# Kernel tuning notes

Measured on AMD Instinct MI355X. Metric: run time of the kernel, lower is better.

## Reference

```python
import jax, jax.numpy as jnp
import numpy as np

N_NODES = 100000
N_EDGES = 800000
EDGE_NAMES = ["ei_connected_to", "ei_ordered_next", "ei_represents", "ei_represented_by",
              "ei_neighboring_vertical", "ei_neighboring_horizontal", "ei_contains",
              "ei_order", "ei_perpendicular"]
AGGRS_L2 = ["sum", "sum", "mean", "mean", "sum", "sum", "mean"]


def _glorot(key, shape):
    fan_in, fan_out = shape[-2], shape[-1]
    s = (2.0 / (fan_in + fan_out)) ** 0.5
    return jax.random.normal(key, shape, dtype=jnp.float32) * s


def setup_inputs() -> dict:
    key = jax.random.key(0)
    ks = iter(jax.random.split(key, 32))
    inp = {"x": jax.random.normal(next(ks), (N_NODES, 6), dtype=jnp.float32)}
    for name in EDGE_NAMES:
        inp[name] = jax.random.randint(next(ks), (2, N_EDGES), 0, N_NODES, dtype=jnp.int32)
    inp.update(
        W0n=_glorot(next(ks), (2, 6, 16)), W0r=_glorot(next(ks), (2, 6, 16)),
        b0=jnp.zeros((2, 16), jnp.float32),
        W1n=_glorot(next(ks), (2, 16, 32)), W1r=_glorot(next(ks), (2, 16, 32)),
        b1=jnp.zeros((2, 32), jnp.float32),
        P1=_glorot(next(ks), (16, 32)), pb1=jnp.zeros((32,), jnp.float32),
        W2n=_glorot(next(ks), (7, 32, 64)), W2r=_glorot(next(ks), (7, 32, 64)),
        b2=jnp.zeros((7, 64), jnp.float32),
        P2=_glorot(next(ks), (32, 64)), pb2=jnp.zeros((64,), jnp.float32),
    )
    return inp


def _hetero_conv(x, edges, aggrs, Wn, Wr, b):
    # Per-relation GraphConv: out_d = aggr(x[src]->dst) @ Wn_r + x @ Wr_r + b_r,
    # summed across relations (HeteroConv aggr='sum'). Loop is over a small fixed
    # set of relation types (structurally distinct), not data dims.
    n = x.shape[0]
    out = jnp.zeros((n, Wn.shape[-1]), x.dtype)
    for i, (ei, aggr) in enumerate(zip(edges, aggrs)):
        src, dst = ei[0], ei[1]
        msg = jax.ops.segment_sum(x[src], dst, num_segments=n)  # scatter-add gather
        if aggr == "mean":
            cnt = jax.ops.segment_sum(jnp.ones_like(dst, dtype=x.dtype), dst, num_segments=n)
            msg = msg / jnp.maximum(cnt, 1.0)[:, None]
        out = out + msg @ Wn[i] + x @ Wr[i] + b[i]
    return out


def reference(x, W0n, W0r, b0, W1n, W1r, b1, P1, pb1, W2n, W2r, b2, P2, pb2,
              ei_connected_to, ei_ordered_next, ei_represents, ei_represented_by,
              ei_neighboring_vertical, ei_neighboring_horizontal, ei_contains,
              ei_order, ei_perpendicular):
    e01 = [ei_connected_to, ei_ordered_next]
    e2 = [ei_represents, ei_represented_by, ei_neighboring_vertical,
          ei_neighboring_horizontal, ei_contains, ei_order, ei_perpendicular]
    # local head: 6 -> 16 (two sum relations)
    h = _hetero_conv(x, e01, ["sum", "sum"], W0n, W0r, b0)
    # residual block 1: 16 -> 32 (same two sum relations, linear residual projection)
    h = jax.nn.relu(_hetero_conv(h, e01, ["sum", "sum"], W1n, W1r, b1) + h @ P1 + pb1)
    # residual block 2: 32 -> 64 (seven relations, sum/mean aggregation)
    h = jax.nn.relu(_hetero_conv(h, e2, AGGRS_L2, W2n, W2r, b2) + h @ P2 + pb2)
    # final elementwise relu from SemanticModule.forward
    return jax.nn.relu(h)
```

## Files before the change

### kernel.cpp

```cpp
#include <hip/hip_runtime.h>

#define NN 100000
#define NE 800000
#define NRG 256
#define SPAN 392
#define CAP 4096
#define NBIN (9 * NRG)

typedef _Float16 f16;
typedef __attribute__((ext_vector_type(4))) _Float16 f16x4;
typedef __attribute__((ext_vector_type(8))) _Float16 f16x8;
typedef __attribute__((ext_vector_type(4))) float f32x4;
typedef __attribute__((ext_vector_type(2))) float f32x2;

#define NTL(p) __builtin_nontemporal_load(p)

struct EPtrs { const int* s[9]; const int* d[9]; };

__global__ __launch_bounds__(256) void prep_weights(
    const float* __restrict__ W0n, const float* __restrict__ W0r, const float* __restrict__ b0,
    const float* __restrict__ W1n, const float* __restrict__ W1r, const float* __restrict__ b1,
    const float* __restrict__ P1,  const float* __restrict__ pb1,
    const float* __restrict__ W2n, const float* __restrict__ W2r, const float* __restrict__ b2,
    const float* __restrict__ P2,  const float* __restrict__ pb2,
    float* __restrict__ wc0, float* __restrict__ bc0,
    float* __restrict__ wc1, float* __restrict__ bc1,
    f16*   __restrict__ b2frag, float* __restrict__ bc2,
    int*   __restrict__ cursor)
{
    int gtid = blockIdx.x * 256 + threadIdx.x;
    int gstr = gridDim.x * 256;

    for (int t = gtid; t < NBIN; t += gstr) cursor[t] = 0;

    for (int t = gtid; t < 18 * 16; t += gstr) {
        int row = t >> 4, col = t & 15;
        float v;
        if (row < 6)       v = W0n[row * 16 + col];
        else if (row < 12) v = W0n[96 + (row - 6) * 16 + col];
        else               v = W0r[(row - 12) * 16 + col] + W0r[96 + (row - 12) * 16 + col];
        wc0[t] = v;
    }
    for (int t = gtid; t < 16; t += gstr) bc0[t] = b0[t] + b0[16 + t];

    for (int t = gtid; t < 48 * 32; t += gstr) {
        int row = t >> 5, col = t & 31;
        float v;
        if (row < 16)      v = W1n[row * 32 + col];
        else if (row < 32) v = W1n[512 + (row - 16) * 32 + col];
        else { int rr = row - 32; v = W1r[rr * 32 + col] + W1r[512 + rr * 32 + col] + P1[rr * 32 + col]; }
        wc1[t] = v;
    }
    for (int t = gtid; t < 32; t += gstr) bc1[t] = b1[t] + b1[32 + t] + pb1[t];

    for (int t = gtid; t < 256 * 64; t += gstr) {
        int j = t & 7, lane = (t >> 3) & 63, ntk = t >> 9;
        int nt = ntk & 3, kt = ntk >> 2;
        int k = kt * 32 + (lane >> 4) * 8 + j;
        int n = nt * 16 + (lane & 15);
        float v;
        if (k < 224) v = W2n[k * 64 + n];
        else {
            int rr = k - 224;
            v = P2[rr * 64 + n];
            #pragma unroll
            for (int r = 0; r < 7; ++r) v += W2r[r * 2048 + rr * 64 + n];
        }
        b2frag[t] = (f16)v;
    }
    for (int t = gtid; t < 64; t += gstr) {
        float v = pb2[t];
        #pragma unroll
        for (int r = 0; r < 7; ++r) v += b2[r * 64 + t];
        bc2[t] = v;
    }
}

__global__ __launch_bounds__(256) void passA(EPtrs ep, int* __restrict__ cursor,
                                             unsigned* __restrict__ binbuf)
{
    int r = blockIdx.y;
    int e0 = blockIdx.x * 4096;
    int cnt = min(4096, NE - e0);
    int tid = threadIdx.x;
    __shared__ int h[NRG];
    __shared__ int bs[NRG];
    __shared__ int cl[NRG];
    __shared__ int gb[NRG];
    __shared__ int wsumA[4];
    __shared__ unsigned pk[4096];
    __shared__ unsigned char pkb[4096];

    h[tid] = 0;
    __syncthreads();

    const int* dp = ep.d[r];
    const int* sp = ep.s[r];
    unsigned wv[16];
    int rgk[16];
    #pragma unroll
    for (int k = 0; k < 16; ++k) {
        int e = e0 + k * 256 + tid;
        rgk[k] = -1;
        if (e < NE) {
            int d = NTL(dp + e);
            int sv = NTL(sp + e);
            int g = d / SPAN;
            int l = d - g * SPAN;
            wv[k] = ((unsigned)l << 17) | (unsigned)sv;
            rgk[k] = g;
            atomicAdd(&h[g], 1);
        }
    }
    __syncthreads();

    int vcnt = h[tid];
    int lane = tid & 63, wid = tid >> 6;
    int incl = vcnt;
    #pragma unroll
    for (int ofs = 1; ofs < 64; ofs <<= 1) {
        int u = __shfl_up(incl, ofs, 64);
        if (lane >= ofs) incl += u;
    }
    if (lane == 63) wsumA[wid] = incl;
    __syncthreads();
    if (tid == 0) {
        int a = wsumA[0], b = wsumA[1], c = wsumA[2];
        wsumA[0] = 0; wsumA[1] = a; wsumA[2] = a + b; wsumA[3] = a + b + c;
    }
    __syncthreads();
    int excl = incl - vcnt + wsumA[wid];
    bs[tid] = excl;
    cl[tid] = excl;
    gb[tid] = (vcnt > 0) ? atomicAdd(&cursor[r * NRG + tid], vcnt) : 0;
    __syncthreads();

    #pragma unroll
    for (int k = 0; k < 16; ++k) {
        if (rgk[k] >= 0) {
            int p = atomicAdd(&cl[rgk[k]], 1);
            pk[p] = wv[k];
            pkb[p] = (unsigned char)rgk[k];
        }
    }
    __syncthreads();

    for (int i = tid; i < cnt; i += 256) {
        int g = pkb[i];
        int pos = gb[g] + (i - bs[g]);
        if (pos < CAP)
            binbuf[((size_t)(r * NRG + g)) * CAP + pos] = pk[i];
    }
}

__global__ __launch_bounds__(256) void passB(const unsigned* __restrict__ binbuf,
                                             const int* __restrict__ cursor,
                                             int* __restrict__ deg, int* __restrict__ off,
                                             int* __restrict__ eidx)
{
    int bin = blockIdx.x;
    int r = bin >> 8, rg = bin & (NRG - 1);
    int lo = rg * SPAN;
    int n_here = min(SPAN, NN - lo);
    int tid = threadIdx.x;
    __shared__ int h[SPAN];
    __shared__ int wsum[4];
    __shared__ int stage[CAP];

    int sz = min(cursor[bin], CAP);
    const unsigned* bp = binbuf + (size_t)bin * CAP;

    for (int i = tid; i < SPAN; i += 256) h[i] = 0;
    __syncthreads();

    unsigned wv[16];
    int rk[16];
    #pragma unroll
    for (int k = 0; k < 16; ++k) {
        int e = tid + k * 256;
        if (e < sz) {
            unsigned w = NTL(bp + e);
            wv[k] = w;
            rk[k] = atomicAdd(&h[w >> 17], 1);
        }
    }
    __syncthreads();

    int i0 = tid * 2;
    int dstash[2];
    int s = 0;
    #pragma unroll
    for (int k = 0; k < 2; ++k) {
        int i = i0 + k;
        int v = (i < SPAN) ? h[i] : 0;
        dstash[k] = v;
        s += v;
    }
    int lane = tid & 63, wid = tid >> 6;
    int incl = s;
    #pragma unroll
    for (int ofs = 1; ofs < 64; ofs <<= 1) {
        int u = __shfl_up(incl, ofs, 64);
        if (lane >= ofs) incl += u;
    }
    if (lane == 63) wsum[wid] = incl;
    __syncthreads();
    if (tid == 0) {
        int a = wsum[0], b = wsum[1], c = wsum[2];
        wsum[0] = 0; wsum[1] = a; wsum[2] = a + b; wsum[3] = a + b + c;
    }
    __syncthreads();
    int run = incl - s + wsum[wid];
    int base = bin * CAP;
    #pragma unroll
    for (int k = 0; k < 2; ++k) {
        int i = i0 + k;
        if (i < SPAN) {
            int v = dstash[k];
            h[i] = run;
            if (i < n_here) {
                deg[r * NN + lo + i] = v;
                off[r * NN + lo + i] = base + run + v;
            }
            run += v;
        }
    }
    __syncthreads();

    #pragma unroll
    for (int k = 0; k < 16; ++k) {
        int e = tid + k * 256;
        if (e < sz) {
            unsigned w = wv[k];
            stage[h[w >> 17] + rk[k]] = (int)(w & 0x1FFFF);
        }
    }
    __syncthreads();
    for (int i = tid; i < sz; i += 256) eidx[base + i] = stage[i];
}

__global__ __launch_bounds__(256) void t0f(const float* __restrict__ x,
                                           const int* __restrict__ deg, const int* __restrict__ off,
                                           const int* __restrict__ eidx,
                                           const float* __restrict__ wc0, const float* __restrict__ bc0,
                                           f16* __restrict__ h0h)
{
    __shared__ float sw[288 + 16];
    for (int t = threadIdx.x; t < 304; t += 256) sw[t] = (t < 288) ? wc0[t] : bc0[t - 288];
    __syncthreads();
    int t = blockIdx.x * 256 + threadIdx.x;
    int node = t >> 2;
    if (node >= NN) return;
    int l = t & 3;
    int r = l >> 1, p = l & 1;

    float m[6] = {0, 0, 0, 0, 0, 0};
    {
        int e1 = off[r * NN + node];
        int e0 = e1 - deg[r * NN + node];
        int e = e0 + p;
        for (; e + 2 < e1; e += 4) {
            int sA = eidx[e], sB = eidx[e + 2];
            const float2* pA = reinterpret_cast<const float2*>(x + (size_t)sA * 6);
            const float2* pB = reinterpret_cast<const float2*>(x + (size_t)sB * 6);
            float2 a0 = pA[0], a1 = pA[1], a2 = pA[2];
            float2 b0 = pB[0], b1 = pB[1], b2 = pB[2];
            m[0] += a0.x + b0.x; m[1] += a0.y + b0.y;
            m[2] += a1.x + b1.x; m[3] += a1.y + b1.y;
            m[4] += a2.x + b2.x; m[5] += a2.y + b2.y;
        }
        if (e < e1) {
            int sA = eidx[e];
            const float2* pA = reinterpret_cast<const float2*>(x + (size_t)sA * 6);
            float2 a0 = pA[0], a1 = pA[1], a2 = pA[2];
            m[0] += a0.x; m[1] += a0.y; m[2] += a1.x; m[3] += a1.y; m[4] += a2.x; m[5] += a2.y;
        }
    }
    float mo[6];
    #pragma unroll
    for (int k = 0; k < 6; ++k) {
        m[k] += __shfl_xor(m[k], 1, 64);
        mo[k] = __shfl_xor(m[k], 2, 64);
    }
    int baseOwn = r * 96, baseOth = (1 - r) * 96;
    float xv[6];
    {
        const float2* xp = reinterpret_cast<const float2*>(x + (size_t)node * 6);
        float2 a = xp[0], b = xp[1], c = xp[2];
        xv[0] = a.x; xv[1] = a.y; xv[2] = b.x; xv[3] = b.y; xv[4] = c.x; xv[5] = c.y;
    }
    int dc = l * 4;
    float acc[4];
    #pragma unroll
    for (int j = 0; j < 4; ++j) acc[j] = sw[288 + dc + j];
    #pragma unroll
    for (int k = 0; k < 6; ++k) {
        #pragma unroll
        for (int j = 0; j < 4; ++j) {
            acc[j] = fmaf(m[k],  sw[baseOwn + k * 16 + dc + j], acc[j]);
            acc[j] = fmaf(mo[k], sw[baseOth + k * 16 + dc + j], acc[j]);
            acc[j] = fmaf(xv[k], sw[192 + k * 16 + dc + j], acc[j]);
        }
    }
    f16x4 o;
    #pragma unroll
    for (int j = 0; j < 4; ++j) o[j] = (f16)acc[j];
    *reinterpret_cast<f16x4*>(h0h + (size_t)node * 16 + dc) = o;
}

__global__ __launch_bounds__(256) void g1t(const int* __restrict__ deg, const int* __restrict__ off,
                                           const int* __restrict__ eidx, const f16* __restrict__ h0h,
                                           const float* __restrict__ wc1, const float* __restrict__ bc1,
                                           f16* __restrict__ h1h, unsigned* __restrict__ h1q)
{
    __shared__ float sw[1536 + 32];
    __shared__ float ms[32][33];
    for (int t = threadIdx.x; t < 1568; t += 256) sw[t] = (t < 1536) ? wc1[t] : bc1[t - 1536];

    int tid = threadIdx.x;
    int nloc = tid >> 3, l = tid & 7;
    int r = l >> 2, dq = l & 3;
    int node = blockIdx.x * 32 + nloc;

    if (node < NN) {
        int e1 = off[r * NN + node];
        int e0 = e1 - deg[r * NN + node];
        float a0 = 0.f, a1 = 0.f, a2 = 0.f, a3 = 0.f;
        int e = e0;
        for (; e + 4 <= e1; e += 4) {
            int sA = eidx[e], sB = eidx[e + 1], sC = eidx[e + 2], sD = eidx[e + 3];
            f16x4 vA = *reinterpret_cast<const f16x4*>(h0h + (size_t)sA * 16 + dq * 4);
            f16x4 vB = *reinterpret_cast<const f16x4*>(h0h + (size_t)sB * 16 + dq * 4);
            f16x4 vC = *reinterpret_cast<const f16x4*>(h0h + (size_t)sC * 16 + dq * 4);
            f16x4 vD = *reinterpret_cast<const f16x4*>(h0h + (size_t)sD * 16 + dq * 4);
            a0 += (float)vA[0] + (float)vB[0] + (float)vC[0] + (float)vD[0];
            a1 += (float)vA[1] + (float)vB[1] + (float)vC[1] + (float)vD[1];
            a2 += (float)vA[2] + (float)vB[2] + (float)vC[2] + (float)vD[2];
            a3 += (float)vA[3] + (float)vB[3] + (float)vC[3] + (float)vD[3];
        }
        for (; e < e1; ++e) {
            f16x4 v = *reinterpret_cast<const f16x4*>(h0h + (size_t)eidx[e] * 16 + dq * 4);
            a0 += (float)v[0]; a1 += (float)v[1]; a2 += (float)v[2]; a3 += (float)v[3];
        }
        ms[nloc][r * 16 + dq * 4 + 0] = a0;
        ms[nloc][r * 16 + dq * 4 + 1] = a1;
        ms[nloc][r * 16 + dq * 4 + 2] = a2;
        ms[nloc][r * 16 + dq * 4 + 3] = a3;
    }
    __syncthreads();
    if (node >= NN) return;

    int c0 = l * 4;
    float acc[4];
    #pragma unroll
    for (int j = 0; j < 4; ++j) acc[j] = sw[1536 + c0 + j];
    #pragma unroll
    for (int k = 0; k < 32; ++k) {
        float s = ms[nloc][k];
        #pragma unroll
        for (int j = 0; j < 4; ++j) acc[j] = fmaf(s, sw[k * 32 + c0 + j], acc[j]);
    }
    {
        const f16x8* hp = reinterpret_cast<const f16x8*>(h0h + (size_t)node * 16);
        f16x8 a = hp[0], b = hp[1];
        #pragma unroll
        for (int k = 0; k < 8; ++k) {
            float s0 = (float)a[k], s1 = (float)b[k];
            #pragma unroll
            for (int j = 0; j < 4; ++j)
                acc[j] = fmaf(s0, sw[(32 + k) * 32 + c0 + j], fmaf(s1, sw[(40 + k) * 32 + c0 + j], acc[j]));
        }
    }
    #pragma unroll
    for (int j = 0; j < 4; ++j) acc[j] = fmaxf(acc[j], 0.f);

    f16x4 o;
    #pragma unroll
    for (int j = 0; j < 4; ++j) o[j] = (f16)acc[j];
    *reinterpret_cast<f16x4*>(h1h + (size_t)node * 32 + c0) = o;

    int w0 = __builtin_amdgcn_cvt_pk_fp8_f32(acc[0], acc[1], 0, false);
    w0 = __builtin_amdgcn_cvt_pk_fp8_f32(acc[2], acc[3], w0, true);
    h1q[(size_t)node * 8 + l] = (unsigned)w0;
}

__global__ __launch_bounds__(256, 8) void g2t2(const int* __restrict__ deg, const int* __restrict__ off,
                                               const int* __restrict__ eidx, const unsigned* __restrict__ h1q,
                                               const f16* __restrict__ h1h, const f16* __restrict__ b2frag,
                                               const float* __restrict__ bc2, float* __restrict__ out)
{
    __shared__ f16 cat[16][264];

    int tid = threadIdx.x;
    int nloc = tid >> 4;
    int lane16 = tid & 15;
    int node = blockIdx.x * 16 + nloc;

    if (lane16 >= 14) {
        int part = lane16 - 14;
        const f16x8* hp = reinterpret_cast<const f16x8*>(h1h + (size_t)node * 32 + part * 16);
        f16x8 v0 = hp[0], v1 = hp[1];
        *reinterpret_cast<f16x8*>(&cat[nloc][224 + part * 16]) = v0;
        *reinterpret_cast<f16x8*>(&cat[nloc][224 + part * 16 + 8]) = v1;
    } else {
        int r = lane16 >> 1;
        int half = lane16 & 1;
        int d = deg[(r + 2) * NN + node];
        int e1 = off[(r + 2) * NN + node];
        int e0 = e1 - d;

        f32x2 acc[8];
        #pragma unroll
        for (int q = 0; q < 8; ++q) acc[q] = (f32x2){0.f, 0.f};

        const uint4* tbl = reinterpret_cast<const uint4*>(h1q);
        int e = e0;
        for (; e + 2 <= e1; e += 2) {
            int sA = eidx[e], sB = eidx[e + 1];
            uint4 qA = tbl[(size_t)sA * 2 + half];
            uint4 qB = tbl[(size_t)sB * 2 + half];
            acc[0] += __builtin_amdgcn_cvt_pk_f32_fp8(qA.x, false);
            acc[1] += __builtin_amdgcn_cvt_pk_f32_fp8(qA.x, true);
            acc[2] += __builtin_amdgcn_cvt_pk_f32_fp8(qA.y, false);
            acc[3] += __builtin_amdgcn_cvt_pk_f32_fp8(qA.y, true);
            acc[4] += __builtin_amdgcn_cvt_pk_f32_fp8(qA.z, false);
            acc[5] += __builtin_amdgcn_cvt_pk_f32_fp8(qA.z, true);
            acc[6] += __builtin_amdgcn_cvt_pk_f32_fp8(qA.w, false);
            acc[7] += __builtin_amdgcn_cvt_pk_f32_fp8(qA.w, true);
            acc[0] += __builtin_amdgcn_cvt_pk_f32_fp8(qB.x, false);
            acc[1] += __builtin_amdgcn_cvt_pk_f32_fp8(qB.x, true);
            acc[2] += __builtin_amdgcn_cvt_pk_f32_fp8(qB.y, false);
            acc[3] += __builtin_amdgcn_cvt_pk_f32_fp8(qB.y, true);
            acc[4] += __builtin_amdgcn_cvt_pk_f32_fp8(qB.z, false);
            acc[5] += __builtin_amdgcn_cvt_pk_f32_fp8(qB.z, true);
            acc[6] += __builtin_amdgcn_cvt_pk_f32_fp8(qB.w, false);
            acc[7] += __builtin_amdgcn_cvt_pk_f32_fp8(qB.w, true);
        }
        if (e < e1) {
            int sA = eidx[e];
            uint4 qA = tbl[(size_t)sA * 2 + half];
            acc[0] += __builtin_amdgcn_cvt_pk_f32_fp8(qA.x, false);
            acc[1] += __builtin_amdgcn_cvt_pk_f32_fp8(qA.x, true);
            acc[2] += __builtin_amdgcn_cvt_pk_f32_fp8(qA.y, false);
            acc[3] += __builtin_amdgcn_cvt_pk_f32_fp8(qA.y, true);
            acc[4] += __builtin_amdgcn_cvt_pk_f32_fp8(qA.z, false);
            acc[5] += __builtin_amdgcn_cvt_pk_f32_fp8(qA.z, true);
            acc[6] += __builtin_amdgcn_cvt_pk_f32_fp8(qA.w, false);
            acc[7] += __builtin_amdgcn_cvt_pk_f32_fp8(qA.w, true);
        }

        float sc = (r == 2 || r == 3 || r == 6) ? (1.0f / (float)max(d, 1)) : 1.0f;
        f16x8 o0, o1;
        #pragma unroll
        for (int q = 0; q < 4; ++q) {
            o0[q * 2 + 0] = (f16)(acc[q][0] * sc);
            o0[q * 2 + 1] = (f16)(acc[q][1] * sc);
            o1[q * 2 + 0] = (f16)(acc[4 + q][0] * sc);
            o1[q * 2 + 1] = (f16)(acc[4 + q][1] * sc);
        }
        *reinterpret_cast<f16x8*>(&cat[nloc][r * 32 + half * 16]) = o0;
        *reinterpret_cast<f16x8*>(&cat[nloc][r * 32 + half * 16 + 8]) = o1;
    }

    int lane = tid & 63, w = tid >> 6;
    int quad = lane >> 4, col0 = lane & 15;
    float bcv = bc2[w * 16 + col0];

    f16x8 bfr[8];
    #pragma unroll
    for (int kt = 0; kt < 8; ++kt)
        bfr[kt] = *reinterpret_cast<const f16x8*>(b2frag + ((size_t)(kt * 4 + w) * 64 + lane) * 8);

    __syncthreads();

    f32x4 acc = (f32x4){0.f, 0.f, 0.f, 0.f};
    #pragma unroll
    for (int kt = 0; kt < 8; ++kt) {
        f16x8 a = *reinterpret_cast<const f16x8*>(&cat[col0][kt * 32 + quad * 8]);
        acc = __builtin_amdgcn_mfma_f32_16x16x32_f16(a, bfr[kt], acc, 0, 0, 0);
    }

    int row0 = blockIdx.x * 16 + quad * 4;
    #pragma unroll
    for (int i = 0; i < 4; ++i)
        out[(size_t)(row0 + i) * 64 + w * 16 + col0] = fmaxf(acc[i] + bcv, 0.f);
}

extern "C" void kernel_launch(void* const* d_in, const int* in_sizes, int n_in,
                              void* d_out, int out_size, void* d_ws, size_t ws_size,
                              hipStream_t stream)
{
    const float* x = (const float*)d_in[0];
    EPtrs ep;
    for (int i = 0; i < 9; ++i) { const int* p = (const int*)d_in[1 + i]; ep.s[i] = p; ep.d[i] = p + NE; }
    const float* W0n = (const float*)d_in[10]; const float* W0r = (const float*)d_in[11];
    const float* b0  = (const float*)d_in[12];
    const float* W1n = (const float*)d_in[13]; const float* W1r = (const float*)d_in[14];
    const float* b1  = (const float*)d_in[15];
    const float* P1  = (const float*)d_in[16]; const float* pb1 = (const float*)d_in[17];
    const float* W2n = (const float*)d_in[18]; const float* W2r = (const float*)d_in[19];
    const float* b2  = (const float*)d_in[20];
    const float* P2  = (const float*)d_in[21]; const float* pb2 = (const float*)d_in[22];
    float* out = (float*)d_out;
    char* ws = (char*)d_ws;

    size_t off_b = 0;
    auto alloc = [&](size_t b) { size_t o = off_b; off_b += (b + 255) & ~(size_t)255; return o; };
    size_t o_wc0 = alloc(288 * 4);   size_t o_bc0 = alloc(16 * 4);
    size_t o_wc1 = alloc(1536 * 4);  size_t o_bc1 = alloc(32 * 4);
    size_t o_b2f = alloc(16384 * 2); size_t o_bc2 = alloc(64 * 4);
    size_t o_h0h = alloc((size_t)NN * 16 * 2);
    size_t o_h1q = alloc((size_t)NN * 32);
    size_t o_h1h = alloc((size_t)NN * 32 * 2);
    size_t o_bin = alloc((size_t)NBIN * CAP * 4);
    size_t o_deg = alloc((size_t)9 * NN * 4);
    size_t o_off = alloc((size_t)9 * NN * 4);
    size_t o_eid = alloc((size_t)NBIN * CAP * 4);
    size_t o_cur = alloc((size_t)NBIN * 4);
    (void)ws_size;

    float* wc0 = (float*)(ws + o_wc0); float* bc0 = (float*)(ws + o_bc0);
    float* wc1 = (float*)(ws + o_wc1); float* bc1 = (float*)(ws + o_bc1);
    f16*   b2f = (f16*)(ws + o_b2f);   float* bc2 = (float*)(ws + o_bc2);
    f16*   h0h = (f16*)(ws + o_h0h);
    unsigned* h1q = (unsigned*)(ws + o_h1q);
    f16*   h1h = (f16*)(ws + o_h1h);
    unsigned* binbuf = (unsigned*)(ws + o_bin);
    int*   deg = (int*)(ws + o_deg);
    int*   offp = (int*)(ws + o_off);
    int*   eid = (int*)(ws + o_eid);
    int*   cur = (int*)(ws + o_cur);

    dim3 B(256);
    prep_weights<<<32, B, 0, stream>>>(W0n, W0r, b0, W1n, W1r, b1, P1, pb1,
                                       W2n, W2r, b2, P2, pb2,
                                       wc0, bc0, wc1, bc1, b2f, bc2, cur);
    passA<<<dim3((NE + 4095) / 4096, 9), B, 0, stream>>>(ep, cur, binbuf);
    passB<<<NBIN, B, 0, stream>>>(binbuf, cur, deg, offp, eid);

    t0f<<<(NN * 4 + 255) / 256, B, 0, stream>>>(x, deg, offp, eid, wc0, bc0, h0h);
    g1t<<<(NN + 31) / 32, B, 0, stream>>>(deg, offp, eid, h0h, wc1, bc1, h1h, h1q);
    g2t2<<<NN / 16, B, 0, stream>>>(deg, offp, eid, h1q, h1h, b2f, bc2, out);
}
```

Baseline: 281.1 us.

## Split g1t gather across lane pairs, drop passA second atomic, split g2t2 launch

passA now keeps the rank returned by the histogram atomic and uses it for placement, removing the second round of shared atomics and the cl array. g1t assigns 16 threads per node instead of 8: each pair of lanes splits one relation's edge list, and the pair combines its partial sums with a shuffle, so each node's gather runs with more parallel loads. g1t now uses 16 nodes per block and computes 2 output columns per thread, with fp8 packing done through a shuffle. g2t2 is launched as two half-size grids over node ranges, adding a base-offset parameter; this adds a launch and gives no clear benefit.

```diff
diff --git a/kernel.cpp b/kernel.cpp
--- a/kernel.cpp
+++ b/kernel.cpp
@@ -8,6 +8,7 @@
 #define NBIN (9 * NRG)
 
 typedef _Float16 f16;
+typedef __attribute__((ext_vector_type(2))) _Float16 f16x2;
 typedef __attribute__((ext_vector_type(4))) _Float16 f16x4;
 typedef __attribute__((ext_vector_type(8))) _Float16 f16x8;
 typedef __attribute__((ext_vector_type(4))) float f32x4;
@@ -85,7 +86,6 @@
     int tid = threadIdx.x;
     __shared__ int h[NRG];
     __shared__ int bs[NRG];
-    __shared__ int cl[NRG];
     __shared__ int gb[NRG];
     __shared__ int wsumA[4];
     __shared__ unsigned pk[4096];
@@ -98,6 +98,7 @@
     const int* sp = ep.s[r];
     unsigned wv[16];
     int rgk[16];
+    int lrk[16];
     #pragma unroll
     for (int k = 0; k < 16; ++k) {
         int e = e0 + k * 256 + tid;
@@ -109,7 +110,7 @@
             int l = d - g * SPAN;
             wv[k] = ((unsigned)l << 17) | (unsigned)sv;
             rgk[k] = g;
-            atomicAdd(&h[g], 1);
+            lrk[k] = atomicAdd(&h[g], 1);
         }
     }
     __syncthreads();
@@ -131,14 +132,13 @@
     __syncthreads();
     int excl = incl - vcnt + wsumA[wid];
     bs[tid] = excl;
-    cl[tid] = excl;
     gb[tid] = (vcnt > 0) ? atomicAdd(&cursor[r * NRG + tid], vcnt) : 0;
     __syncthreads();
 
     #pragma unroll
     for (int k = 0; k < 16; ++k) {
         if (rgk[k] >= 0) {
-            int p = atomicAdd(&cl[rgk[k]], 1);
+            int p = bs[rgk[k]] + lrk[k];
             pk[p] = wv[k];
             pkb[p] = (unsigned char)rgk[k];
         }
@@ -314,51 +314,52 @@
                                            f16* __restrict__ h1h, unsigned* __restrict__ h1q)
 {
     __shared__ float sw[1536 + 32];
-    __shared__ float ms[32][33];
+    __shared__ float ms[16][33];
     for (int t = threadIdx.x; t < 1568; t += 256) sw[t] = (t < 1536) ? wc1[t] : bc1[t - 1536];
 
     int tid = threadIdx.x;
-    int nloc = tid >> 3, l = tid & 7;
-    int r = l >> 2, dq = l & 3;
-    int node = blockIdx.x * 32 + nloc;
-
-    if (node < NN) {
+    int nloc = tid >> 4, l = tid & 15;
+    int r = l >> 3, dq = (l >> 1) & 3, p = l & 1;
+    int node = blockIdx.x * 16 + nloc;
+
+    {
         int e1 = off[r * NN + node];
         int e0 = e1 - deg[r * NN + node];
         float a0 = 0.f, a1 = 0.f, a2 = 0.f, a3 = 0.f;
-        int e = e0;
-        for (; e + 4 <= e1; e += 4) {
-            int sA = eidx[e], sB = eidx[e + 1], sC = eidx[e + 2], sD = eidx[e + 3];
+        int e = e0 + p;
+        for (; e + 2 < e1; e += 4) {
+            int sA = eidx[e], sB = eidx[e + 2];
             f16x4 vA = *reinterpret_cast<const f16x4*>(h0h + (size_t)sA * 16 + dq * 4);
             f16x4 vB = *reinterpret_cast<const f16x4*>(h0h + (size_t)sB * 16 + dq * 4);
-            f16x4 vC = *reinterpret_cast<const f16x4*>(h0h + (size_t)sC * 16 + dq * 4);
-            f16x4 vD = *reinterpret_cast<const f16x4*>(h0h + (size_t)sD * 16 + dq * 4);
-            a0 += (float)vA[0] + (float)vB[0] + (float)vC[0] + (float)vD[0];
-            a1 += (float)vA[1] + (float)vB[1] + (float)vC[1] + (float)vD[1];
-            a2 += (float)vA[2] + (float)vB[2] + (float)vC[2] + (float)vD[2];
-            a3 += (float)vA[3] + (float)vB[3] + (float)vC[3] + (float)vD[3];
-        }
-        for (; e < e1; ++e) {
+            a0 += (float)vA[0] + (float)vB[0];
+            a1 += (float)vA[1] + (float)vB[1];
+            a2 += (float)vA[2] + (float)vB[2];
+            a3 += (float)vA[3] + (float)vB[3];
+        }
+        if (e < e1) {
             f16x4 v = *reinterpret_cast<const f16x4*>(h0h + (size_t)eidx[e] * 16 + dq * 4);
             a0 += (float)v[0]; a1 += (float)v[1]; a2 += (float)v[2]; a3 += (float)v[3];
         }
-        ms[nloc][r * 16 + dq * 4 + 0] = a0;
-        ms[nloc][r * 16 + dq * 4 + 1] = a1;
-        ms[nloc][r * 16 + dq * 4 + 2] = a2;
-        ms[nloc][r * 16 + dq * 4 + 3] = a3;
-    }
-    __syncthreads();
-    if (node >= NN) return;
-
-    int c0 = l * 4;
-    float acc[4];
-    #pragma unroll
-    for (int j = 0; j < 4; ++j) acc[j] = sw[1536 + c0 + j];
+        a0 += __shfl_xor(a0, 1, 64);
+        a1 += __shfl_xor(a1, 1, 64);
+        a2 += __shfl_xor(a2, 1, 64);
+        a3 += __shfl_xor(a3, 1, 64);
+        if (p == 0) {
+            ms[nloc][r * 16 + dq * 4 + 0] = a0;
+            ms[nloc][r * 16 + dq * 4 + 1] = a1;
+            ms[nloc][r * 16 + dq * 4 + 2] = a2;
+            ms[nloc][r * 16 + dq * 4 + 3] = a3;
+        }
+    }
+    __syncthreads();
+
+    int c0 = l * 2;
+    float acc0 = sw[1536 + c0], acc1 = sw[1536 + c0 + 1];
     #pragma unroll
     for (int k = 0; k < 32; ++k) {
         float s = ms[nloc][k];
-        #pragma unroll
-        for (int j = 0; j < 4; ++j) acc[j] = fmaf(s, sw[k * 32 + c0 + j], acc[j]);
+        acc0 = fmaf(s, sw[k * 32 + c0], acc0);
+        acc1 = fmaf(s, sw[k * 32 + c0 + 1], acc1);
     }
     {
         const f16x8* hp = reinterpret_cast<const f16x8*>(h0h + (size_t)node * 16);
@@ -366,35 +367,38 @@
         #pragma unroll
         for (int k = 0; k < 8; ++k) {
             float s0 = (float)a[k], s1 = (float)b[k];
-            #pragma unroll
-            for (int j = 0; j < 4; ++j)
-                acc[j] = fmaf(s0, sw[(32 + k) * 32 + c0 + j], fmaf(s1, sw[(40 + k) * 32 + c0 + j], acc[j]));
-        }
-    }
-    #pragma unroll
-    for (int j = 0; j < 4; ++j) acc[j] = fmaxf(acc[j], 0.f);
-
-    f16x4 o;
-    #pragma unroll
-    for (int j = 0; j < 4; ++j) o[j] = (f16)acc[j];
-    *reinterpret_cast<f16x4*>(h1h + (size_t)node * 32 + c0) = o;
-
-    int w0 = __builtin_amdgcn_cvt_pk_fp8_f32(acc[0], acc[1], 0, false);
-    w0 = __builtin_amdgcn_cvt_pk_fp8_f32(acc[2], acc[3], w0, true);
-    h1q[(size_t)node * 8 + l] = (unsigned)w0;
+            acc0 = fmaf(s0, sw[(32 + k) * 32 + c0], fmaf(s1, sw[(40 + k) * 32 + c0], acc0));
+            acc1 = fmaf(s0, sw[(32 + k) * 32 + c0 + 1], fmaf(s1, sw[(40 + k) * 32 + c0 + 1], acc1));
+        }
+    }
+    acc0 = fmaxf(acc0, 0.f);
+    acc1 = fmaxf(acc1, 0.f);
+
+    f16x2 o;
+    o[0] = (f16)acc0; o[1] = (f16)acc1;
+    *reinterpret_cast<f16x2*>(h1h + (size_t)node * 32 + c0) = o;
+
+    float pa0 = __shfl_xor(acc0, 1, 64);
+    float pa1 = __shfl_xor(acc1, 1, 64);
+    if (p == 0) {
+        int w = __builtin_amdgcn_cvt_pk_fp8_f32(acc0, acc1, 0, false);
+        w = __builtin_amdgcn_cvt_pk_fp8_f32(pa0, pa1, w, true);
+        h1q[(size_t)node * 8 + (l >> 1)] = (unsigned)w;
+    }
 }
 
 __global__ __launch_bounds__(256, 8) void g2t2(const int* __restrict__ deg, const int* __restrict__ off,
                                                const int* __restrict__ eidx, const unsigned* __restrict__ h1q,
                                                const f16* __restrict__ h1h, const f16* __restrict__ b2frag,
-                                               const float* __restrict__ bc2, float* __restrict__ out)
+                                               const float* __restrict__ bc2, float* __restrict__ out,
+                                               int nbase)
 {
     __shared__ f16 cat[16][264];
 
     int tid = threadIdx.x;
     int nloc = tid >> 4;
     int lane16 = tid & 15;
-    int node = blockIdx.x * 16 + nloc;
+    int node = nbase + blockIdx.x * 16 + nloc;
 
     if (lane16 >= 14) {
         int part = lane16 - 14;
@@ -480,7 +484,7 @@
         acc = __builtin_amdgcn_mfma_f32_16x16x32_f16(a, bfr[kt], acc, 0, 0, 0);
     }
 
-    int row0 = blockIdx.x * 16 + quad * 4;
+    int row0 = nbase + blockIdx.x * 16 + quad * 4;
     #pragma unroll
     for (int i = 0; i < 4; ++i)
         out[(size_t)(row0 + i) * 64 + w * 16 + col0] = fmaxf(acc[i] + bcv, 0.f);
@@ -539,6 +543,7 @@
     passB<<<NBIN, B, 0, stream>>>(binbuf, cur, deg, offp, eid);
 
     t0f<<<(NN * 4 + 255) / 256, B, 0, stream>>>(x, deg, offp, eid, wc0, bc0, h0h);
-    g1t<<<(NN + 31) / 32, B, 0, stream>>>(deg, offp, eid, h0h, wc1, bc1, h1h, h1q);
-    g2t2<<<NN / 16, B, 0, stream>>>(deg, offp, eid, h1q, h1h, b2f, bc2, out);
-}
+    g1t<<<NN / 16, B, 0, stream>>>(deg, offp, eid, h0h, wc1, bc1, h1h, h1q);
+    g2t2<<<NN / 32, B, 0, stream>>>(deg, offp, eid, h1q, h1h, b2f, bc2, out, 0);
+    g2t2<<<NN / 32, B, 0, stream>>>(deg, offp, eid, h1q, h1h, b2f, bc2, out, NN / 2);
+}
```

Result: slower. 292.9 us (+4.2%).
